# Performance work log

Measured on AMD Instinct MI355X. Metric: run time of the kernel, lower is better.

Reference implementation:

```python
import jax, jax.numpy as jnp
import numpy as np

B, T_IN, F, U = 4096, 256, 32, 64
OUT_STEPS = 24


def _lstm_step(x, h, c, W, R, b):
    # Keras LSTMCell: gates z = x@W + h@R + b, split as [i, f, g, o]
    z = x @ W + h @ R + b  # [B, 4U]
    i, f, g, o = jnp.split(z, 4, axis=-1)
    i = jax.nn.sigmoid(i)
    f = jax.nn.sigmoid(f)
    g = jnp.tanh(g)
    o = jax.nn.sigmoid(o)
    c_new = f * c + i * g
    h_new = o * jnp.tanh(c_new)
    return h_new, c_new


def setup_inputs() -> dict:
    key = jax.random.key(0)
    ks = jax.random.split(key, 9)
    s_in = 1.0 / np.sqrt(F)
    s_hid = 1.0 / np.sqrt(U)
    return {
        "inputs": jax.random.normal(ks[0], (B, T_IN, F), jnp.float32),
        "W1": jax.random.normal(ks[1], (F, 4 * U), jnp.float32) * s_in,
        "U1": jax.random.normal(ks[2], (U, 4 * U), jnp.float32) * s_hid,
        "b1": jnp.zeros((4 * U,), jnp.float32),
        "W2": jax.random.normal(ks[3], (F, 4 * U), jnp.float32) * s_in,
        "U2": jax.random.normal(ks[4], (U, 4 * U), jnp.float32) * s_hid,
        "b2": jnp.zeros((4 * U,), jnp.float32),
        "Wd": jax.random.normal(ks[5], (U, F), jnp.float32) * s_hid,
        "bd": jnp.zeros((F,), jnp.float32),
    }


def reference(inputs, W1, U1, b1, W2, U2, b2, Wd, bd):
    batch = inputs.shape[0]
    units = U1.shape[0]
    h0 = jnp.zeros((batch, units), inputs.dtype)
    c0 = jnp.zeros((batch, units), inputs.dtype)

    # ---- warmup: run lstm_cell_warmup over the input sequence ----
    def warm_step(carry, x_t):
        h, c = carry
        h, c = _lstm_step(x_t, h, c, W1, U1, b1)
        return (h, c), None

    (h, c), _ = jax.lax.scan(warm_step, (h0, c0), jnp.swapaxes(inputs, 0, 1))
    pred0 = h @ Wd + bd  # [B, F]

    def dec_step(carry, _):
        pred, h, c = carry
        h, c = _lstm_step(pred, h, c, W2, U2, b2)
        pred = h @ Wd + bd
        return (pred, h, c), pred

    _, preds_rest = jax.lax.scan(dec_step, (pred0, h, c), None, length=OUT_STEPS - 1)
    preds = jnp.concatenate([pred0[None], preds_rest], axis=0)  # [T_out, B, F]
    return jnp.transpose(preds, (1, 0, 2))  # [B, T_out, F]
```

## Files before the change

kernel.cpp:

```cpp
#include <hip/hip_runtime.h>
#include <math.h>

#define T_STEPS 256
#define Fdim 32
#define Udim 64
#define G4 256
#define OUT_STEPS 24
#define ROWS 16
#define NBLK 256
#define NTHR 512
#define HBS 72
#define CHUNK 32
#define NCHUNK 8
#define LOG2E 1.4426950408889634f

typedef __attribute__((ext_vector_type(8))) short short8;
typedef __attribute__((ext_vector_type(4))) float f32x4;

__device__ __forceinline__ short f2bf(float f) {
    union { float f; unsigned u; } v; v.f = f;
    unsigned r = v.u + 0x7FFFu + ((v.u >> 16) & 1u);
    return (short)(r >> 16);
}
__device__ __forceinline__ float bf2f(short s) {
    union { unsigned u; float f; } v; v.u = ((unsigned)(unsigned short)s) << 16;
    return v.f;
}
__device__ __forceinline__ float frcp(float v) { return __builtin_amdgcn_rcpf(v); }
__device__ __forceinline__ float fexp2(float v) { return __builtin_amdgcn_exp2f(v); }

__device__ __forceinline__ unsigned pkbf(float lo, float hi) {
    unsigned r;
    asm("v_cvt_pk_bf16_f32 %0, %1, %2" : "=v"(r) : "v"(lo), "v"(hi));
    return r;
}

__device__ __forceinline__ int swz(int col, int row) { return col ^ ((row & 8) << 2); }

__device__ __forceinline__ float cell_h(const f32x4 a, float& cst) {
    float A  = fexp2(-a[0]);
    float Bv = fexp2(a[2]);
    float rf = frcp(1.0f + fexp2(-a[1]));
    float ig = (Bv - 1.0f) * frcp((1.0f + A) * (1.0f + Bv));
    cst = fmaf(cst, rf, ig);
    float C  = fexp2(-a[3]);
    float D  = fexp2(2.0f * LOG2E * cst);
    return (D - 1.0f) * frcp((1.0f + C) * (1.0f + D));
}

#define BAR() asm volatile("s_waitcnt lgkmcnt(0)\n\ts_barrier" ::: "memory")

#define MFMA __builtin_amdgcn_mfma_f32_16x16x32_bf16

__global__ __launch_bounds__(NTHR, 1)
void lstm_v7(const float* __restrict__ x,
             const float* __restrict__ W1, const float* __restrict__ U1, const float* __restrict__ b1,
             const float* __restrict__ W2, const float* __restrict__ U2, const float* __restrict__ b2,
             const float* __restrict__ Wd, const float* __restrict__ bd,
             float* __restrict__ out)
{
    __shared__ __align__(16) short hb[2][ROWS][HBS];
    __shared__ __align__(16) short xs[CHUNK][ROWS][HBS];
    __shared__ float WdL[Udim * Fdim];

    const int tid = threadIdx.x;
    const int l   = tid & 63;
    const int w   = tid >> 6;
    const int q   = l >> 4;
    const int m   = l & 15;
    const int brow = blockIdx.x * ROWS;

    const int f4 = tid & 7;
    const int tt = (tid >> 3) & 31;
    const int r0 = tid >> 8;
    float4 pf[8];
#pragma unroll
    for (int i = 0; i < 8; ++i)
        pf[i] = *(const float4*)&x[((size_t)(brow + r0 + 2 * i) * T_STEPS + tt) * Fdim + f4 * 4];

    short8 wa1[2][3], wa2[2][3];
    f32x4 bs1[2], bs2[2];
#pragma unroll
    for (int nt = 0; nt < 2; ++nt) {
        const int unit_a = w * 8 + (m >> 2) * 2 + nt;
        const int gate_a = m & 3;
        const int col = gate_a * 64 + unit_a;
        const float sA = (gate_a == 2) ? 2.0f * LOG2E : LOG2E;
#pragma unroll
        for (int kt = 0; kt < 3; ++kt) {
            short8 fa, fb;
#pragma unroll
            for (int j = 0; j < 8; ++j) {
                const int k = kt * 32 + q * 8 + j;
                float v1 = (k < Udim) ? U1[k * G4 + col] : W1[(k - Udim) * G4 + col];
                float v2 = (k < Udim) ? U2[k * G4 + col] : W2[(k - Udim) * G4 + col];
                fa[j] = f2bf(v1 * sA);
                fb[j] = f2bf(v2 * sA);
            }
            wa1[nt][kt] = fa;
            wa2[nt][kt] = fb;
        }
        const int unit_d = w * 8 + q * 2 + nt;
#pragma unroll
        for (int g = 0; g < 4; ++g) {
            const float sD = (g == 2) ? 2.0f * LOG2E : LOG2E;
            bs1[nt][g] = b1[g * 64 + unit_d] * sD;
            bs2[nt][g] = b2[g * 64 + unit_d] * sD;
        }
    }

    const int sr = tid >> 5;
    const int sc = tid & 31;
    const float bdv = bd[sc];
    const int hw = w * 8 + q * 2;
    const int bswz = (m & 8) << 2;

    for (int idx = tid; idx < 2 * ROWS * HBS; idx += NTHR) ((short*)hb)[idx] = 0;
    for (int idx = tid; idx < Udim * Fdim; idx += NTHR) WdL[idx] = Wd[idx];
    float cst[2] = {0.f, 0.f};

    for (int c = 0; c < NCHUNK; ++c) {
#pragma unroll
        for (int i = 0; i < 8; ++i) {
            const int row = r0 + 2 * i;
            uint2 pk;
            pk.x = pkbf(pf[i].x, pf[i].y);
            pk.y = pkbf(pf[i].z, pf[i].w);
            *(uint2*)&xs[tt][row][swz(f4 * 4, row)] = pk;
        }
        if (c + 1 < NCHUNK) {
#pragma unroll
            for (int i = 0; i < 8; ++i)
                pf[i] = *(const float4*)&x[((size_t)(brow + r0 + 2 * i) * T_STEPS + ((c + 1) * CHUNK + tt)) * Fdim + f4 * 4];
        }
        BAR();

        short8 b2p = *(const short8*)&xs[0][m][(q * 8) ^ bswz];

#pragma unroll 2
        for (int t2 = 0; t2 < CHUNK; ++t2) {
            const int p = t2 & 1;

            const short8 b2v = b2p;
            const short8 b0  = *(const short8*)&hb[p][m][(q * 8) ^ bswz];
            const short8 b1v = *(const short8*)&hb[p][m][(32 + q * 8) ^ bswz];

            f32x4 a0 = MFMA(wa1[0][2], b2v, bs1[0], 0, 0, 0);
            f32x4 a1 = MFMA(wa1[1][2], b2v, bs1[1], 0, 0, 0);
            a0 = MFMA(wa1[0][0], b0, a0, 0, 0, 0);
            a1 = MFMA(wa1[1][0], b0, a1, 0, 0, 0);
            a0 = MFMA(wa1[0][1], b1v, a0, 0, 0, 0);
            a1 = MFMA(wa1[1][1], b1v, a1, 0, 0, 0);

            const float h0 = cell_h(a0, cst[0]);
            const float h1 = cell_h(a1, cst[1]);
            *(unsigned*)&hb[1 - p][m][hw ^ bswz] = pkbf(h0, h1);
            if (t2 + 1 < CHUNK)
                b2p = *(const short8*)&xs[t2 + 1][m][(q * 8) ^ bswz];
            BAR();
        }
    }

    short8 b0p, b1p;
    {
        float acc = bdv;
#pragma unroll
        for (int kb = 0; kb < 8; ++kb) {
            short8 h8 = *(const short8*)&hb[0][sr][swz(kb * 8, sr)];
#pragma unroll
            for (int j = 0; j < 8; ++j)
                acc = fmaf(bf2f(h8[j]), WdL[(kb * 8 + j) * Fdim + sc], acc);
        }
        out[(size_t)(brow + sr) * (OUT_STEPS * Fdim) + sc] = acc;
        xs[0][sr][swz(sc, sr)] = f2bf(acc);
        b0p = *(const short8*)&hb[0][m][(q * 8) ^ bswz];
        b1p = *(const short8*)&hb[0][m][(32 + q * 8) ^ bswz];
    }
    BAR();

    int dp = 0;
    for (int s = 1; s < OUT_STEPS; ++s) {
        const short8 b2v = *(const short8*)&xs[0][m][(q * 8) ^ bswz];

        f32x4 a0 = MFMA(wa2[0][0], b0p, bs2[0], 0, 0, 0);
        f32x4 a1 = MFMA(wa2[1][0], b0p, bs2[1], 0, 0, 0);
        a0 = MFMA(wa2[0][1], b1p, a0, 0, 0, 0);
        a1 = MFMA(wa2[1][1], b1p, a1, 0, 0, 0);
        a0 = MFMA(wa2[0][2], b2v, a0, 0, 0, 0);
        a1 = MFMA(wa2[1][2], b2v, a1, 0, 0, 0);

        const float h0 = cell_h(a0, cst[0]);
        const float h1 = cell_h(a1, cst[1]);
        *(unsigned*)&hb[1 - dp][m][hw ^ bswz] = pkbf(h0, h1);
        BAR();

        float dacc = bdv;
#pragma unroll
        for (int kb = 0; kb < 8; ++kb) {
            short8 h8 = *(const short8*)&hb[1 - dp][sr][swz(kb * 8, sr)];
#pragma unroll
            for (int j = 0; j < 8; ++j)
                dacc = fmaf(bf2f(h8[j]), WdL[(kb * 8 + j) * Fdim + sc], dacc);
        }
        out[(size_t)(brow + sr) * (OUT_STEPS * Fdim) + s * Fdim + sc] = dacc;
        xs[0][sr][swz(sc, sr)] = f2bf(dacc);
        b0p = *(const short8*)&hb[1 - dp][m][(q * 8) ^ bswz];
        b1p = *(const short8*)&hb[1 - dp][m][(32 + q * 8) ^ bswz];
        BAR();
        dp = 1 - dp;
    }
}

extern "C" void kernel_launch(void* const* d_in, const int* in_sizes, int n_in,
                              void* d_out, int out_size, void* d_ws, size_t ws_size,
                              hipStream_t stream) {
    (void)in_sizes; (void)n_in; (void)out_size; (void)d_ws; (void)ws_size;
    const float* x  = (const float*)d_in[0];
    const float* W1 = (const float*)d_in[1];
    const float* U1 = (const float*)d_in[2];
    const float* b1 = (const float*)d_in[3];
    const float* W2 = (const float*)d_in[4];
    const float* U2 = (const float*)d_in[5];
    const float* b2 = (const float*)d_in[6];
    const float* Wd = (const float*)d_in[7];
    const float* bd = (const float*)d_in[8];
    float* out = (float*)d_out;

    lstm_v7<<<dim3(NBLK), dim3(NTHR), 0, stream>>>(
        x, W1, U1, b1, W2, U2, b2, Wd, bd, out);
}
```

Measured before the change: 309.4 us.

## Use MFMA for dense projection, preload x chunk into registers, drop swizzle

```diff
diff --git a/kernel.cpp b/kernel.cpp
--- a/kernel.cpp
+++ b/kernel.cpp
@@ -10,8 +10,8 @@
 #define NBLK 256
 #define NTHR 512
 #define HBS 72
-#define CHUNK 32
-#define NCHUNK 8
+#define CHUNK 16
+#define NCHUNK 16
 #define LOG2E 1.4426950408889634f
 
 typedef __attribute__((ext_vector_type(8))) short short8;
@@ -34,8 +34,6 @@
     asm("v_cvt_pk_bf16_f32 %0, %1, %2" : "=v"(r) : "v"(lo), "v"(hi));
     return r;
 }
-
-__device__ __forceinline__ int swz(int col, int row) { return col ^ ((row & 8) << 2); }
 
 __device__ __forceinline__ float cell_h(const f32x4 a, float& cst) {
     float A  = fexp2(-a[0]);
@@ -52,16 +50,15 @@
 
 #define MFMA __builtin_amdgcn_mfma_f32_16x16x32_bf16
 
-__global__ __launch_bounds__(NTHR, 1)
-void lstm_v7(const float* __restrict__ x,
-             const float* __restrict__ W1, const float* __restrict__ U1, const float* __restrict__ b1,
-             const float* __restrict__ W2, const float* __restrict__ U2, const float* __restrict__ b2,
-             const float* __restrict__ Wd, const float* __restrict__ bd,
-             float* __restrict__ out)
+__global__ __launch_bounds__(NTHR, 2)
+void lstm_v10(const float* __restrict__ x,
+              const float* __restrict__ W1, const float* __restrict__ U1, const float* __restrict__ b1,
+              const float* __restrict__ W2, const float* __restrict__ U2, const float* __restrict__ b2,
+              const float* __restrict__ Wd, const float* __restrict__ bd,
+              float* __restrict__ out)
 {
     __shared__ __align__(16) short hb[2][ROWS][HBS];
     __shared__ __align__(16) short xs[CHUNK][ROWS][HBS];
-    __shared__ float WdL[Udim * Fdim];
 
     const int tid = threadIdx.x;
     const int l   = tid & 63;
@@ -70,13 +67,13 @@
     const int m   = l & 15;
     const int brow = blockIdx.x * ROWS;
 
-    const int f4 = tid & 7;
-    const int tt = (tid >> 3) & 31;
-    const int r0 = tid >> 8;
-    float4 pf[8];
-#pragma unroll
-    for (int i = 0; i < 8; ++i)
-        pf[i] = *(const float4*)&x[((size_t)(brow + r0 + 2 * i) * T_STEPS + tt) * Fdim + f4 * 4];
+    const int f4  = tid & 7;
+    const int tt  = (tid >> 3) & 15;
+    const int xr0 = tid >> 7;
+    float4 pf[4];
+#pragma unroll
+    for (int i = 0; i < 4; ++i)
+        pf[i] = *(const float4*)&x[((size_t)(brow + xr0 + 4 * i) * T_STEPS + tt) * Fdim + f4 * 4];
 
     short8 wa1[2][3], wa2[2][3];
     f32x4 bs1[2], bs2[2];
@@ -109,44 +106,60 @@
         }
     }
 
-    const int sr = tid >> 5;
-    const int sc = tid & 31;
-    const float bdv = bd[sc];
+    short8 wdh[2], wdlo[2];
+    f32x4 bdC;
+    {
+        const int wsel = (w < 2) ? w : 0;
+#pragma unroll
+        for (int kt = 0; kt < 2; ++kt) {
+            short8 fh, fl;
+#pragma unroll
+            for (int j = 0; j < 8; ++j) {
+                const float v = Wd[(kt * 32 + q * 8 + j) * Fdim + 16 * wsel + m];
+                const short hi = f2bf(v);
+                fh[j] = hi;
+                fl[j] = f2bf(v - bf2f(hi));
+            }
+            wdh[kt] = fh;
+            wdlo[kt] = fl;
+        }
+#pragma unroll
+        for (int g = 0; g < 4; ++g) bdC[g] = bd[16 * wsel + q * 4 + g];
+    }
+
     const int hw = w * 8 + q * 2;
-    const int bswz = (m & 8) << 2;
-
     for (int idx = tid; idx < 2 * ROWS * HBS; idx += NTHR) ((short*)hb)[idx] = 0;
-    for (int idx = tid; idx < Udim * Fdim; idx += NTHR) WdL[idx] = Wd[idx];
     float cst[2] = {0.f, 0.f};
 
     for (int c = 0; c < NCHUNK; ++c) {
 #pragma unroll
-        for (int i = 0; i < 8; ++i) {
-            const int row = r0 + 2 * i;
+        for (int i = 0; i < 4; ++i) {
             uint2 pk;
             pk.x = pkbf(pf[i].x, pf[i].y);
             pk.y = pkbf(pf[i].z, pf[i].w);
-            *(uint2*)&xs[tt][row][swz(f4 * 4, row)] = pk;
+            *(uint2*)&xs[tt][xr0 + 4 * i][f4 * 4] = pk;
         }
         if (c + 1 < NCHUNK) {
 #pragma unroll
-            for (int i = 0; i < 8; ++i)
-                pf[i] = *(const float4*)&x[((size_t)(brow + r0 + 2 * i) * T_STEPS + ((c + 1) * CHUNK + tt)) * Fdim + f4 * 4];
+            for (int i = 0; i < 4; ++i)
+                pf[i] = *(const float4*)&x[((size_t)(brow + xr0 + 4 * i) * T_STEPS + ((c + 1) * CHUNK + tt)) * Fdim + f4 * 4];
         }
         BAR();
 
-        short8 b2p = *(const short8*)&xs[0][m][(q * 8) ^ bswz];
-
-#pragma unroll 2
+        short8 xf[CHUNK];
+#pragma unroll
+        for (int t = 0; t < CHUNK; ++t)
+            xf[t] = *(const short8*)&xs[t][m][q * 8];
+
+#pragma unroll
         for (int t2 = 0; t2 < CHUNK; ++t2) {
             const int p = t2 & 1;
 
-            const short8 b2v = b2p;
-            const short8 b0  = *(const short8*)&hb[p][m][(q * 8) ^ bswz];
-            const short8 b1v = *(const short8*)&hb[p][m][(32 + q * 8) ^ bswz];
-
-            f32x4 a0 = MFMA(wa1[0][2], b2v, bs1[0], 0, 0, 0);
-            f32x4 a1 = MFMA(wa1[1][2], b2v, bs1[1], 0, 0, 0);
+            const short8 b0  = *(const short8*)&hb[p][m][q * 8];
+            const short8 b1v = *(const short8*)&hb[p][m][32 + q * 8];
+
+            f32x4 a0 = MFMA(wa1[0][2], xf[t2], bs1[0], 0, 0, 0);
+            f32x4 a1 = MFMA(wa1[1][2], xf[t2], bs1[1], 0, 0, 0);
             a0 = MFMA(wa1[0][0], b0, a0, 0, 0, 0);
             a1 = MFMA(wa1[1][0], b0, a1, 0, 0, 0);
             a0 = MFMA(wa1[0][1], b1v, a0, 0, 0, 0);
@@ -154,33 +167,29 @@
 
             const float h0 = cell_h(a0, cst[0]);
             const float h1 = cell_h(a1, cst[1]);
-            *(unsigned*)&hb[1 - p][m][hw ^ bswz] = pkbf(h0, h1);
-            if (t2 + 1 < CHUNK)
-                b2p = *(const short8*)&xs[t2 + 1][m][(q * 8) ^ bswz];
+            *(unsigned*)&hb[1 - p][m][hw] = pkbf(h0, h1);
             BAR();
         }
     }
 
-    short8 b0p, b1p;
-    {
-        float acc = bdv;
-#pragma unroll
-        for (int kb = 0; kb < 8; ++kb) {
-            short8 h8 = *(const short8*)&hb[0][sr][swz(kb * 8, sr)];
-#pragma unroll
-            for (int j = 0; j < 8; ++j)
-                acc = fmaf(bf2f(h8[j]), WdL[(kb * 8 + j) * Fdim + sc], acc);
-        }
-        out[(size_t)(brow + sr) * (OUT_STEPS * Fdim) + sc] = acc;
-        xs[0][sr][swz(sc, sr)] = f2bf(acc);
-        b0p = *(const short8*)&hb[0][m][(q * 8) ^ bswz];
-        b1p = *(const short8*)&hb[0][m][(32 + q * 8) ^ bswz];
+    short8 b0p = *(const short8*)&hb[0][m][q * 8];
+    short8 b1p = *(const short8*)&hb[0][m][32 + q * 8];
+    if (w < 2) {
+        f32x4 pz = MFMA(wdh[0], b0p, bdC, 0, 0, 0);
+        pz = MFMA(wdh[1], b1p, pz, 0, 0, 0);
+        pz = MFMA(wdlo[0], b0p, pz, 0, 0, 0);
+        pz = MFMA(wdlo[1], b1p, pz, 0, 0, 0);
+        *(f32x4*)&out[(size_t)(brow + m) * (OUT_STEPS * Fdim) + 16 * w + q * 4] = pz;
+        uint2 fp;
+        fp.x = pkbf(pz[0], pz[1]);
+        fp.y = pkbf(pz[2], pz[3]);
+        *(uint2*)&xs[0][m][16 * w + q * 4] = fp;
     }
     BAR();
 
     int dp = 0;
     for (int s = 1; s < OUT_STEPS; ++s) {
-        const short8 b2v = *(const short8*)&xs[0][m][(q * 8) ^ bswz];
+        const short8 b2v = *(const short8*)&xs[0][m][q * 8];
 
         f32x4 a0 = MFMA(wa2[0][0], b0p, bs2[0], 0, 0, 0);
         f32x4 a1 = MFMA(wa2[1][0], b0p, bs2[1], 0, 0, 0);
@@ -191,21 +200,22 @@
 
         const float h0 = cell_h(a0, cst[0]);
         const float h1 = cell_h(a1, cst[1]);
-        *(unsigned*)&hb[1 - dp][m][hw ^ bswz] = pkbf(h0, h1);
+        *(unsigned*)&hb[1 - dp][m][hw] = pkbf(h0, h1);
         BAR();
 
-        float dacc = bdv;
-#pragma unroll
-        for (int kb = 0; kb < 8; ++kb) {
-            short8 h8 = *(const short8*)&hb[1 - dp][sr][swz(kb * 8, sr)];
-#pragma unroll
-            for (int j = 0; j < 8; ++j)
-                dacc = fmaf(bf2f(h8[j]), WdL[(kb * 8 + j) * Fdim + sc], dacc);
-        }
-        out[(size_t)(brow + sr) * (OUT_STEPS * Fdim) + s * Fdim + sc] = dacc;
-        xs[0][sr][swz(sc, sr)] = f2bf(dacc);
-        b0p = *(const short8*)&hb[1 - dp][m][(q * 8) ^ bswz];
-        b1p = *(const short8*)&hb[1 - dp][m][(32 + q * 8) ^ bswz];
+        b0p = *(const short8*)&hb[1 - dp][m][q * 8];
+        b1p = *(const short8*)&hb[1 - dp][m][32 + q * 8];
+        if (w < 2) {
+            f32x4 pz = MFMA(wdh[0], b0p, bdC, 0, 0, 0);
+            pz = MFMA(wdh[1], b1p, pz, 0, 0, 0);
+            pz = MFMA(wdlo[0], b0p, pz, 0, 0, 0);
+            pz = MFMA(wdlo[1], b1p, pz, 0, 0, 0);
+            *(f32x4*)&out[(size_t)(brow + m) * (OUT_STEPS * Fdim) + s * Fdim + 16 * w + q * 4] = pz;
+            uint2 fp;
+            fp.x = pkbf(pz[0], pz[1]);
+            fp.y = pkbf(pz[2], pz[3]);
+            *(uint2*)&xs[0][m][16 * w + q * 4] = fp;
+        }
         BAR();
         dp = 1 - dp;
     }
@@ -226,6 +236,6 @@
     const float* bd = (const float*)d_in[8];
     float* out = (float*)d_out;
 
-    lstm_v7<<<dim3(NBLK), dim3(NTHR), 0, stream>>>(
+    lstm_v10<<<dim3(NBLK), dim3(NTHR), 0, stream>>>(
         x, W1, U1, b1, W2, U2, b2, Wd, bd, out);
 }
```

New measurement: 277.5 us. -10.3%, faster.
